# Optimization experiments

Hardware: AMD Instinct MI355X
Metric: run time of the kernel (lower is better)

The kernel has to match this reference:

```python
import jax, jax.numpy as jnp
import numpy as np

B, N, C = 4, 1024, 256
E = 65536
HID = 256  # LAYERS = [256, 256, 256]

def _linear_init(key, out_dim, in_dim):
    kw, kb = jax.random.split(key)
    s = 1.0 / np.sqrt(in_dim)
    W = jax.random.uniform(kw, (out_dim, in_dim), jnp.float32, -s, s)
    b = jax.random.uniform(kb, (out_dim,), jnp.float32, -s, s)
    return W, b

def setup_inputs() -> dict:
    key = jax.random.key(0)
    ks = jax.random.split(key, 5)
    pooled_features = jax.random.normal(ks[0], (B, N, C), jnp.float32)
    edge_index = jax.random.randint(ks[1], (2, E), 0, B * N)  # [src; dst]
    W1, b1 = _linear_init(ks[2], HID, 2 * C)
    W2, b2 = _linear_init(ks[3], HID, 2 * HID)
    W3, b3 = _linear_init(ks[4], HID, 2 * HID)
    return {"pooled_features": pooled_features, "edge_index": edge_index,
            "W1": W1, "b1": b1, "W2": W2, "b2": b2, "W3": W3, "b3": b3}

def _edge_conv(x, src, dst, num_nodes, W, b):
    # PyG EdgeConv: x_j = x[src], x_i = x[dst]; msg = relu(fc([x_j - x_i, x_i]));
    # aggr='max' scatters messages onto dst nodes.
    x_i = x[dst]                                   # [E, d]
    x_j = x[src]                                   # [E, d]
    msg = jnp.concatenate([x_j - x_i, x_i], axis=-1)  # [E, 2d]
    msg = jax.nn.relu(msg @ W.T + b)               # [E, out]
    out = jax.ops.segment_max(msg, dst, num_segments=num_nodes)
    # empty segments -> -inf; PyG fills with 0, and relu messages are >= 0
    return jnp.maximum(out, 0.0)

def reference(pooled_features, edge_index, W1, b1, W2, b2, W3, b3):
    b_, n_, c_ = pooled_features.shape
    num_nodes = b_ * n_
    x = pooled_features.reshape(num_nodes, c_)
    src, dst = edge_index[0], edge_index[1]
    feats = [x]
    for W, bb in ((W1, b1), (W2, b2), (W3, b3)):
        x = _edge_conv(x, src, dst, num_nodes, W, bb)
        feats.append(x)
    related_features = jnp.concatenate(feats, axis=-1)  # [num_nodes, 1024]
    return related_features
```

## Files before the change

kernel.cpp:

```cpp
#include <hip/hip_runtime.h>


#define NODES 4096
#define EDGES 65536
#define OSTR 1024
#define DEGCAP 64

typedef __attribute__((ext_vector_type(8))) short bf16x8;
typedef __attribute__((ext_vector_type(4))) float f32x4;

__device__ __forceinline__ unsigned short f2bf(float f) {
    unsigned int x = __float_as_uint(f);
    return (unsigned short)((x + 0x7fff + ((x >> 16) & 1)) >> 16);
}
__device__ __forceinline__ float bf2f(unsigned short u) {
    return __uint_as_float(((unsigned int)u) << 16);
}

__device__ __forceinline__ void gemm_phase(int l, const short* Alds,
                                           const short* __restrict__ Wp,
                                           const float* __restrict__ bias,
                                           unsigned short* __restrict__ UWu,
                                           float* __restrict__ UWw,
                                           int b, int t) {
    const int wv = t >> 6, lane = t & 63;
    const int lm = lane & 15, kq = lane >> 4;
    const int nhalf = wv >> 3, sub = wv & 7;
    f32x4 acc0 = (f32x4){0.f, 0.f, 0.f, 0.f};
    f32x4 acc1 = (f32x4){0.f, 0.f, 0.f, 0.f};
    const short* ap = Alds + lm * 264 + kq * 8;
    const short* bp = Wp + (size_t)l * 131072
                         + (size_t)(nhalf * 256 + sub * 32 + lm) * 256 + kq * 8;
#pragma unroll
    for (int ks = 0; ks < 8; ++ks) {
        const int ko = ks * 32;
        bf16x8 a  = *(const bf16x8*)(ap + ko);
        bf16x8 q0 = *(const bf16x8*)(bp + ko);
        bf16x8 q1 = *(const bf16x8*)(bp + 16 * 256 + ko);
        acc0 = __builtin_amdgcn_mfma_f32_16x16x32_bf16(a, q0, acc0, 0, 0, 0);
        acc1 = __builtin_amdgcn_mfma_f32_16x16x32_bf16(a, q1, acc1, 0, 0, 0);
    }
    unsigned short* UW = UWu + (size_t)(l & 1) * NODES * 256;
#pragma unroll
    for (int nt2 = 0; nt2 < 2; ++nt2) {
        int nc = sub * 32 + nt2 * 16 + lm;
        f32x4 av = nt2 ? acc1 : acc0;
        if (nhalf == 0) {
#pragma unroll
            for (int p = 0; p < 4; ++p)
                UW[(size_t)(b * 16 + kq * 4 + p) * 256 + nc] = f2bf(av[p]);
        } else {
            float bc = bias[nc];
#pragma unroll
            for (int p = 0; p < 4; ++p)
                UWw[(size_t)(b * 16 + kq * 4 + p) * 256 + nc] = av[p] + bc;
        }
    }
}

__device__ __forceinline__ void edge_phase(int l,
                                           const unsigned short* __restrict__ UWu,
                                           const float* __restrict__ UWw,
                                           const int* __restrict__ cursor,
                                           const int* __restrict__ srcS,
                                           float* __restrict__ out,
                                           short* AldsW, int b, int t) {
    const int wv = t >> 6, lane = t & 63;
    const int i = b * 16 + wv;
    int deg = cursor[i]; if (deg > DEGCAP) deg = DEGCAP;
    const int beg = i * DEGCAP, end = beg + deg;
    const unsigned short* UW = UWu + (size_t)(l & 1) * NODES * 256;
    const float NEG = -3.4e38f;
    float mx0 = NEG, mx1 = NEG, mx2 = NEG, mx3 = NEG;
    int e = beg;
    for (; e + 8 <= end; e += 8) {
        int4 sa = *(const int4*)(srcS + e);
        int4 sb = *(const int4*)(srcS + e + 4);
        ushort4 v0 = *(const ushort4*)(UW + (size_t)sa.x * 256 + lane * 4);
        ushort4 v1 = *(const ushort4*)(UW + (size_t)sa.y * 256 + lane * 4);
        ushort4 v2 = *(const ushort4*)(UW + (size_t)sa.z * 256 + lane * 4);
        ushort4 v3 = *(const ushort4*)(UW + (size_t)sa.w * 256 + lane * 4);
        ushort4 v4 = *(const ushort4*)(UW + (size_t)sb.x * 256 + lane * 4);
        ushort4 v5 = *(const ushort4*)(UW + (size_t)sb.y * 256 + lane * 4);
        ushort4 v6 = *(const ushort4*)(UW + (size_t)sb.z * 256 + lane * 4);
        ushort4 v7 = *(const ushort4*)(UW + (size_t)sb.w * 256 + lane * 4);
        mx0 = fmaxf(mx0, fmaxf(fmaxf(bf2f(v0.x), bf2f(v1.x)), fmaxf(bf2f(v2.x), bf2f(v3.x))));
        mx0 = fmaxf(mx0, fmaxf(fmaxf(bf2f(v4.x), bf2f(v5.x)), fmaxf(bf2f(v6.x), bf2f(v7.x))));
        mx1 = fmaxf(mx1, fmaxf(fmaxf(bf2f(v0.y), bf2f(v1.y)), fmaxf(bf2f(v2.y), bf2f(v3.y))));
        mx1 = fmaxf(mx1, fmaxf(fmaxf(bf2f(v4.y), bf2f(v5.y)), fmaxf(bf2f(v6.y), bf2f(v7.y))));
        mx2 = fmaxf(mx2, fmaxf(fmaxf(bf2f(v0.z), bf2f(v1.z)), fmaxf(bf2f(v2.z), bf2f(v3.z))));
        mx2 = fmaxf(mx2, fmaxf(fmaxf(bf2f(v4.z), bf2f(v5.z)), fmaxf(bf2f(v6.z), bf2f(v7.z))));
        mx3 = fmaxf(mx3, fmaxf(fmaxf(bf2f(v0.w), bf2f(v1.w)), fmaxf(bf2f(v2.w), bf2f(v3.w))));
        mx3 = fmaxf(mx3, fmaxf(fmaxf(bf2f(v4.w), bf2f(v5.w)), fmaxf(bf2f(v6.w), bf2f(v7.w))));
    }
    for (; e + 4 <= end; e += 4) {
        int4 sa = *(const int4*)(srcS + e);
        ushort4 v0 = *(const ushort4*)(UW + (size_t)sa.x * 256 + lane * 4);
        ushort4 v1 = *(const ushort4*)(UW + (size_t)sa.y * 256 + lane * 4);
        ushort4 v2 = *(const ushort4*)(UW + (size_t)sa.z * 256 + lane * 4);
        ushort4 v3 = *(const ushort4*)(UW + (size_t)sa.w * 256 + lane * 4);
        mx0 = fmaxf(mx0, fmaxf(fmaxf(bf2f(v0.x), bf2f(v1.x)), fmaxf(bf2f(v2.x), bf2f(v3.x))));
        mx1 = fmaxf(mx1, fmaxf(fmaxf(bf2f(v0.y), bf2f(v1.y)), fmaxf(bf2f(v2.y), bf2f(v3.y))));
        mx2 = fmaxf(mx2, fmaxf(fmaxf(bf2f(v0.z), bf2f(v1.z)), fmaxf(bf2f(v2.z), bf2f(v3.z))));
        mx3 = fmaxf(mx3, fmaxf(fmaxf(bf2f(v0.w), bf2f(v1.w)), fmaxf(bf2f(v2.w), bf2f(v3.w))));
    }
    for (; e < end; ++e) {
        int s = srcS[e];
        ushort4 v = *(const ushort4*)(UW + (size_t)s * 256 + lane * 4);
        mx0 = fmaxf(mx0, bf2f(v.x)); mx1 = fmaxf(mx1, bf2f(v.y));
        mx2 = fmaxf(mx2, bf2f(v.z)); mx3 = fmaxf(mx3, bf2f(v.w));
    }
    float4 w4 = *(const float4*)(UWw + (size_t)i * 256 + lane * 4);
    f32x4 r;
    r[0] = fmaxf(mx0 + w4.x, 0.0f);
    r[1] = fmaxf(mx1 + w4.y, 0.0f);
    r[2] = fmaxf(mx2 + w4.z, 0.0f);
    r[3] = fmaxf(mx3 + w4.w, 0.0f);
    *(f32x4*)(out + (size_t)i * OSTR + (l + 1) * 256 + lane * 4) = r;
    if (AldsW) {
        ushort4 rb;
        rb.x = f2bf(r[0]); rb.y = f2bf(r[1]); rb.z = f2bf(r[2]); rb.w = f2bf(r[3]);
        *(ushort4*)(AldsW + wv * 264 + lane * 4) = rb;
    }
}

__global__ __launch_bounds__(256) void k_prep(const float* __restrict__ x0,
                                              const int* __restrict__ srcIdx,
                                              const int* __restrict__ dstIdx,
                                              const float* __restrict__ W0,
                                              const float* __restrict__ W1,
                                              const float* __restrict__ W2,
                                              float* __restrict__ out,
                                              short* __restrict__ Wp,
                                              int* __restrict__ cursor,
                                              int* __restrict__ srcS) {
    int tid = blockIdx.x * 256 + threadIdx.x;
    f32x4 v = ((const f32x4*)x0)[tid];
    ((f32x4*)out)[(size_t)(tid >> 6) * 256 + (tid & 63)] = v;
    for (int q = tid; q < 393216; q += 262144) {
        int layer = q >> 17, idx = q & 131071;
        const float* W = layer == 0 ? W0 : (layer == 1 ? W1 : W2);
        int n2 = idx >> 8, c = idx & 255;
        float wv2 = (n2 < 256) ? W[n2 * 512 + c]
                               : W[(n2 - 256) * 512 + 256 + c] - W[(n2 - 256) * 512 + c];
        Wp[q] = (short)f2bf(wv2);
    }
    if (tid < EDGES) {
        int d = dstIdx[tid];
        int p = atomicAdd(&cursor[d], 1);
        if (p < DEGCAP) srcS[d * DEGCAP + p] = srcIdx[tid];
    }
}

__global__ __launch_bounds__(1024, 4) void k_g0(const float* __restrict__ x0,
                                                const short* __restrict__ Wp,
                                                const float* __restrict__ B0,
                                                unsigned short* __restrict__ UWu,
                                                float* __restrict__ UWw) {
    __shared__ __align__(16) short Alds[16 * 264];
    const int t = threadIdx.x, b = blockIdx.x;
    {
        int row = t >> 6, c4 = t & 63;
        f32x4 v = *((const f32x4*)x0 + (size_t)(b * 16 + row) * 64 + c4);
        ushort4 hb;
        hb.x = f2bf(v[0]); hb.y = f2bf(v[1]); hb.z = f2bf(v[2]); hb.w = f2bf(v[3]);
        *(ushort4*)(Alds + row * 264 + c4 * 4) = hb;
    }
    __syncthreads();
    gemm_phase(0, Alds, Wp, B0, UWu, UWw, b, t);
}

__global__ __launch_bounds__(1024, 4) void k_eg(int l,
                                                const short* __restrict__ Wp,
                                                const float* __restrict__ biasN,
                                                unsigned short* __restrict__ UWu,
                                                float* __restrict__ UWw,
                                                const int* __restrict__ cursor,
                                                const int* __restrict__ srcS,
                                                float* __restrict__ out) {
    __shared__ __align__(16) short Alds[16 * 264];
    const int t = threadIdx.x, b = blockIdx.x;
    edge_phase(l, UWu, UWw, cursor, srcS, out, Alds, b, t);
    __syncthreads();
    gemm_phase(l + 1, Alds, Wp, biasN, UWu, UWw, b, t);
}

__global__ __launch_bounds__(1024, 4) void k_e2(const unsigned short* __restrict__ UWu,
                                                const float* __restrict__ UWw,
                                                const int* __restrict__ cursor,
                                                const int* __restrict__ srcS,
                                                float* __restrict__ out) {
    const int t = threadIdx.x, b = blockIdx.x;
    edge_phase(2, UWu, UWw, cursor, srcS, out, (short*)nullptr, b, t);
}

extern "C" void kernel_launch(void* const* d_in, const int* in_sizes, int n_in,
                              void* d_out, int out_size, void* d_ws, size_t ws_size,
                              hipStream_t stream) {
    const float* x0 = (const float*)d_in[0];
    const int* ei = (const int*)d_in[1];
    const int* srcIdx = ei;
    const int* dstIdx = ei + EDGES;
    float* out = (float*)d_out;

    char* w = (char*)d_ws;
    unsigned short* UWu = (unsigned short*)w;
    float* UWw = (float*)(w + 4194304);
    short* Wp = (short*)(w + 8388608);
    int* srcS = (int*)(w + 9175040);
    int* cursor = (int*)(w + 10223616);

    (void)hipMemsetAsync((void*)cursor, 0, 16384, stream);

    const float* W0 = (const float*)d_in[2]; const float* B0 = (const float*)d_in[3];
    const float* W1 = (const float*)d_in[4]; const float* B1 = (const float*)d_in[5];
    const float* W2 = (const float*)d_in[6]; const float* B2 = (const float*)d_in[7];

    k_prep<<<1024, 256, 0, stream>>>(x0, srcIdx, dstIdx, W0, W1, W2, out, Wp, cursor, srcS);
    k_g0<<<256, 1024, 0, stream>>>(x0, Wp, B0, UWu, UWw);
    k_eg<<<256, 1024, 0, stream>>>(0, Wp, B1, UWu, UWw, cursor, srcS, out);
    k_eg<<<256, 1024, 0, stream>>>(1, Wp, B2, UWu, UWw, cursor, srcS, out);
    k_e2<<<256, 1024, 0, stream>>>(UWu, UWw, cursor, srcS, out);
}
```

Baseline: 132.3 us.

## Drop memset launch and move edge bucketing and x0 copy into first GEMM kernel

Replaces the hipMemsetAsync of the per-node cursor array with a zeroing store inside the prep kernel, which shrinks to 512 blocks and now only packs weights. The x0 copy into the output and the atomic bucketing of edges by destination move into k_g0, overlapping them with the layer-0 GEMM load phase. This removes one stream operation and reworks which kernel does which piece of setup. Bucketing stays in a separate launch from the prep kernel that zeroes the cursors, so ordering still holds.

```diff
diff --git a/kernel.cpp b/kernel.cpp
--- a/kernel.cpp
+++ b/kernel.cpp
@@ -124,47 +124,49 @@
     }
 }
 
-__global__ __launch_bounds__(256) void k_prep(const float* __restrict__ x0,
-                                              const int* __restrict__ srcIdx,
-                                              const int* __restrict__ dstIdx,
-                                              const float* __restrict__ W0,
+__global__ __launch_bounds__(256) void k_prep(const float* __restrict__ W0,
                                               const float* __restrict__ W1,
                                               const float* __restrict__ W2,
-                                              float* __restrict__ out,
                                               short* __restrict__ Wp,
-                                              int* __restrict__ cursor,
-                                              int* __restrict__ srcS) {
+                                              int* __restrict__ cursor) {
     int tid = blockIdx.x * 256 + threadIdx.x;
-    f32x4 v = ((const f32x4*)x0)[tid];
-    ((f32x4*)out)[(size_t)(tid >> 6) * 256 + (tid & 63)] = v;
-    for (int q = tid; q < 393216; q += 262144) {
-        int layer = q >> 17, idx = q & 131071;
-        const float* W = layer == 0 ? W0 : (layer == 1 ? W1 : W2);
-        int n2 = idx >> 8, c = idx & 255;
+    const float* Ws[3] = {W0, W1, W2};
+#pragma unroll
+    for (int layer = 0; layer < 3; ++layer) {
+        const float* W = Ws[layer];
+        int n2 = tid >> 8, c = tid & 255;
         float wv2 = (n2 < 256) ? W[n2 * 512 + c]
                                : W[(n2 - 256) * 512 + 256 + c] - W[(n2 - 256) * 512 + c];
-        Wp[q] = (short)f2bf(wv2);
-    }
-    if (tid < EDGES) {
-        int d = dstIdx[tid];
-        int p = atomicAdd(&cursor[d], 1);
-        if (p < DEGCAP) srcS[d * DEGCAP + p] = srcIdx[tid];
-    }
+        Wp[layer * 131072 + tid] = (short)f2bf(wv2);
+    }
+    if (tid < NODES) cursor[tid] = 0;
 }
 
 __global__ __launch_bounds__(1024, 4) void k_g0(const float* __restrict__ x0,
+                                                const int* __restrict__ srcIdx,
+                                                const int* __restrict__ dstIdx,
                                                 const short* __restrict__ Wp,
                                                 const float* __restrict__ B0,
                                                 unsigned short* __restrict__ UWu,
-                                                float* __restrict__ UWw) {
+                                                float* __restrict__ UWw,
+                                                int* __restrict__ cursor,
+                                                int* __restrict__ srcS,
+                                                float* __restrict__ out) {
     __shared__ __align__(16) short Alds[16 * 264];
     const int t = threadIdx.x, b = blockIdx.x;
+    const int gtid = b * 1024 + t;
     {
         int row = t >> 6, c4 = t & 63;
         f32x4 v = *((const f32x4*)x0 + (size_t)(b * 16 + row) * 64 + c4);
+        ((f32x4*)out)[(size_t)(b * 16 + row) * 256 + c4] = v;
         ushort4 hb;
         hb.x = f2bf(v[0]); hb.y = f2bf(v[1]); hb.z = f2bf(v[2]); hb.w = f2bf(v[3]);
         *(ushort4*)(Alds + row * 264 + c4 * 4) = hb;
+    }
+    if (gtid < EDGES) {
+        int d = dstIdx[gtid];
+        int p = atomicAdd(&cursor[d], 1);
+        if (p < DEGCAP) srcS[d * DEGCAP + p] = srcIdx[gtid];
     }
     __syncthreads();
     gemm_phase(0, Alds, Wp, B0, UWu, UWw, b, t);
@@ -210,14 +212,12 @@
     int* srcS = (int*)(w + 9175040);
     int* cursor = (int*)(w + 10223616);
 
-    (void)hipMemsetAsync((void*)cursor, 0, 16384, stream);
-
     const float* W0 = (const float*)d_in[2]; const float* B0 = (const float*)d_in[3];
     const float* W1 = (const float*)d_in[4]; const float* B1 = (const float*)d_in[5];
     const float* W2 = (const float*)d_in[6]; const float* B2 = (const float*)d_in[7];
 
-    k_prep<<<1024, 256, 0, stream>>>(x0, srcIdx, dstIdx, W0, W1, W2, out, Wp, cursor, srcS);
-    k_g0<<<256, 1024, 0, stream>>>(x0, Wp, B0, UWu, UWw);
+    k_prep<<<512, 256, 0, stream>>>(W0, W1, W2, Wp, cursor);
+    k_g0<<<256, 1024, 0, stream>>>(x0, srcIdx, dstIdx, Wp, B0, UWu, UWw, cursor, srcS, out);
     k_eg<<<256, 1024, 0, stream>>>(0, Wp, B1, UWu, UWw, cursor, srcS, out);
     k_eg<<<256, 1024, 0, stream>>>(1, Wp, B2, UWu, UWw, cursor, srcS, out);
     k_e2<<<256, 1024, 0, stream>>>(UWu, UWw, cursor, srcS, out);
```

Result: no change. 131.0 us (median of 2 runs) (-1.0%).
